# Kernel optimization log

Measured on AMD Instinct MI355X. Metric: run time of the kernel, lower is better.

The kernel has to match this reference:

```python
import jax, jax.numpy as jnp
import numpy as np

N_NODES = 100000
N_EDGES = 1600000
IN_DIM = 256
OUT_DIM = 128
SELF_LOOP_W = 2.0  # improved=True


def setup_inputs() -> dict:
    key = jax.random.key(0)
    ks = jax.random.split(key, 9)
    x = jax.random.normal(ks[0], (N_NODES, IN_DIM), dtype=jnp.float32)
    edge_index = jax.random.randint(ks[1], (2, N_EDGES), 0, N_NODES, dtype=jnp.int64)
    edge_weight = jax.random.uniform(ks[2], (N_EDGES,), dtype=jnp.float32)
    s1 = 1.0 / np.sqrt(IN_DIM)
    s2 = 1.0 / np.sqrt(OUT_DIM)
    W1 = jax.random.normal(ks[3], (IN_DIM, OUT_DIM), dtype=jnp.float32) * s1
    b1 = jnp.zeros((OUT_DIM,), dtype=jnp.float32)
    W_mu = jax.random.normal(ks[4], (OUT_DIM, OUT_DIM), dtype=jnp.float32) * s2
    b_mu = jnp.zeros((OUT_DIM,), dtype=jnp.float32)
    W_var = jax.random.normal(ks[5], (OUT_DIM, OUT_DIM), dtype=jnp.float32) * s2
    b_var = jnp.zeros((OUT_DIM,), dtype=jnp.float32)
    return {"x": x, "edge_index": edge_index, "edge_weight": edge_weight,
            "W1": W1, "b1": b1, "W_mu": W_mu, "b_mu": b_mu,
            "W_var": W_var, "b_var": b_var}


def _gcn_norm(edge_index, edge_weight, num_nodes):
    # add self loops with fill value 2.0 (improved=True), then symmetric norm
    loop = jnp.arange(num_nodes, dtype=edge_index.dtype)
    row = jnp.concatenate([edge_index[0], loop])
    col = jnp.concatenate([edge_index[1], loop])
    ew = jnp.concatenate([edge_weight,
                          jnp.full((num_nodes,), SELF_LOOP_W, dtype=edge_weight.dtype)])
    deg = jax.ops.segment_sum(ew, col, num_segments=num_nodes)
    dis = jnp.where(deg > 0, jax.lax.rsqrt(jnp.where(deg > 0, deg, 1.0)), 0.0)
    norm = dis[row] * ew * dis[col]
    return row, col, norm


def _gcn_conv(x, row, col, norm, W, b, num_nodes):
    xw = x @ W                      # [N, out]
    msg = xw[row] * norm[:, None]   # [E+N, out] per-edge messages
    out = jax.ops.segment_sum(msg, col, num_segments=num_nodes)
    return out + b


def reference(x, edge_index, edge_weight, W1, b1, W_mu, b_mu, W_var, b_var):
    n = x.shape[0]
    row, col, norm = _gcn_norm(edge_index, edge_weight, n)
    feat = jax.nn.relu(_gcn_conv(x, row, col, norm, W1, b1, n))
    mu = _gcn_conv(feat, row, col, norm, W_mu, b_mu, n)
    var = _gcn_conv(feat, row, col, norm, W_var, b_var, n)
    return (mu, var)
```

## Files before the change

kernel.cpp:

```cpp
#include <hip/hip_runtime.h>
#include <hip/hip_bf16.h>

#define CDIV(a,b) (((a)+(b)-1)/(b))

typedef __attribute__((ext_vector_type(8))) short short8;
typedef __attribute__((ext_vector_type(4))) float f32x4;

static __device__ inline short f2bf(float f) {
    union { __hip_bfloat16 h; short s; } u;
    u.h = __float2bfloat16(f);
    return u.s;
}
static __device__ inline ushort f2bfu(float f) { return (ushort)f2bf(f); }
static __device__ inline float bfu_lo(uint v) { return __uint_as_float(v << 16); }
static __device__ inline float bfu_hi(uint v) { return __uint_as_float(v & 0xffff0000u); }


__global__ __launch_bounds__(512) void k_init(const float* __restrict__ W1,
                                              short* __restrict__ W1t,
                                              const float* __restrict__ Wmu,
                                              const float* __restrict__ Wvar,
                                              short* __restrict__ Wcat) {
    int i = blockIdx.x * 512 + threadIdx.x;
    if (i < 128 * 256) {
        int k = i % 256, col = i / 256;
        W1t[i] = f2bf(W1[(size_t)k * 128 + col]);
    } else if (i < 2 * 128 * 256) {
        int j = i - 128 * 256;
        int k = j & 127, col = j >> 7;
        float v = (col < 128) ? Wmu[(size_t)k * 128 + col] : Wvar[(size_t)k * 128 + (col - 128)];
        Wcat[j] = f2bf(v);
    }
}


__global__ __launch_bounds__(512) void k_bhist(const int* __restrict__ coli,
                                               int* __restrict__ bhist,
                                               int E, int chunk, int nbk) {
    __shared__ int h[256];
    int b = blockIdx.x, t = threadIdx.x, nblk = gridDim.x;
    for (int i = t; i < nbk; i += 512) h[i] = 0;
    __syncthreads();
    int e0 = b * chunk, e1 = min(E, e0 + chunk);
    for (int e = e0 + t; e < e1; e += 512)
        atomicAdd(&h[coli[e] >> 9], 1);
    __syncthreads();
    for (int i = t; i < nbk; i += 512)
        bhist[i * nblk + b] = h[i];
}

__global__ __launch_bounds__(256) void kscanA(const int* __restrict__ in,
                                              int* __restrict__ out,
                                              int* __restrict__ part, int n) {
    int t = threadIdx.x;
    int base = blockIdx.x * 1024 + t * 4;
    int v0 = (base + 0 < n) ? in[base + 0] : 0;
    int v1 = (base + 1 < n) ? in[base + 1] : 0;
    int v2 = (base + 2 < n) ? in[base + 2] : 0;
    int v3 = (base + 3 < n) ? in[base + 3] : 0;
    int tsum = v0 + v1 + v2 + v3;
    int lane = t & 63, wv = t >> 6;
    int val = tsum;
    #pragma unroll
    for (int d = 1; d < 64; d <<= 1) {
        int u = __shfl_up(val, d, 64);
        if (lane >= d) val += u;
    }
    __shared__ int ws[4];
    if (lane == 63) ws[wv] = val;
    __syncthreads();
    int woff = 0;
    #pragma unroll
    for (int i = 0; i < 4; ++i) if (i < wv) woff += ws[i];
    int excl = woff + val - tsum;
    if (base + 0 < n) out[base + 0] = excl;  excl += v0;
    if (base + 1 < n) out[base + 1] = excl;  excl += v1;
    if (base + 2 < n) out[base + 2] = excl;  excl += v2;
    if (base + 3 < n) out[base + 3] = excl;
    if (t == 255) part[blockIdx.x] = woff + val;
}

__global__ __launch_bounds__(128) void kscanB(int* part, int nb) {
    int t = threadIdx.x;
    int v = (t < nb) ? part[t] : 0;
    int lane = t & 63, wv = t >> 6;
    int val = v;
    #pragma unroll
    for (int d = 1; d < 64; d <<= 1) {
        int u = __shfl_up(val, d, 64);
        if (lane >= d) val += u;
    }
    __shared__ int ws[2];
    if (lane == 63) ws[wv] = val;
    __syncthreads();
    int woff = (wv == 1) ? ws[0] : 0;
    if (t < nb) part[t] = woff + val - v;
}

__global__ __launch_bounds__(256) void kscanC(int* __restrict__ out,
                                              const int* __restrict__ part, int n) {
    int i = blockIdx.x * 256 + threadIdx.x;
    if (i < n) out[i] += part[i >> 10];
}

__global__ __launch_bounds__(512) void k_bucket(const int* __restrict__ rowi,
                                                const int* __restrict__ coli,
                                                const float* __restrict__ ew,
                                                const int* __restrict__ excl,
                                                int2* __restrict__ bxw,
                                                int E, int chunk, int nbk) {
    __shared__ int cur[256];
    int b = blockIdx.x, t = threadIdx.x, nblk = gridDim.x;
    for (int i = t; i < nbk; i += 512) cur[i] = 0;
    __syncthreads();
    int e0 = b * chunk, e1 = min(E, e0 + chunk);
    for (int e = e0 + t; e < e1; e += 512) {
        int c = coli[e];
        int bk = c >> 9;
        int pos = excl[bk * nblk + b] + atomicAdd(&cur[bk], 1);
        bxw[pos] = make_int2(((c & 511) << 17) | rowi[e], __float_as_int(ew[e]));
    }
}

__global__ __launch_bounds__(512) void k_fine2(const int2* __restrict__ bxw,
                                               const int* __restrict__ excl,
                                               int* __restrict__ row_ptr,
                                               float* __restrict__ dis,
                                               int E, int nblk, int n) {
    __shared__ int cnt[512], ews[512];
    int bk = blockIdx.x, t = threadIdx.x;
    cnt[t] = 0; ews[t] = 0;
    __syncthreads();
    int s0 = excl[bk * nblk];
    int s1 = (bk + 1 < gridDim.x) ? excl[(bk + 1) * nblk] : E;
    for (int p = s0 + t; p < s1; p += 512) {
        int2 u = bxw[p];
        int cl = u.x >> 17;
        atomicAdd(&cnt[cl], 1);
        int q = (int)(__int_as_float(u.y) * 16777216.0f + 0.5f);
        atomicAdd(&ews[cl], q);
    }
    __syncthreads();
    int v = cnt[t];
    int lane = t & 63, wv = t >> 6;
    int val = v;
    #pragma unroll
    for (int d = 1; d < 64; d <<= 1) {
        int u = __shfl_up(val, d, 64);
        if (lane >= d) val += u;
    }
    __shared__ int ws2[8];
    if (lane == 63) ws2[wv] = val;
    __syncthreads();
    int woff = 0;
    #pragma unroll
    for (int i = 0; i < 8; ++i) if (i < wv) woff += ws2[i];
    int lexcl = woff + val - v;
    int c = bk * 512 + t;
    if (c < n) {
        row_ptr[c] = s0 + lexcl;
        dis[c] = rsqrtf(2.0f + (float)ews[t] * (1.0f / 16777216.0f));
    }
    if (bk == 0 && t == 0) row_ptr[n] = E;
}

__global__ __launch_bounds__(512) void k_place(const int2* __restrict__ bxw,
                                               const int* __restrict__ excl,
                                               const int* __restrict__ row_ptr,
                                               const float* __restrict__ dis,
                                               int2* __restrict__ csr,
                                               int E, int nblk, int n) {
    __shared__ int cur[512];
    int bk = blockIdx.x, t = threadIdx.x;
    cur[t] = 0;
    __syncthreads();
    int s0 = excl[bk * nblk];
    int s1 = (bk + 1 < gridDim.x) ? excl[(bk + 1) * nblk] : E;
    int cbase = bk * 512;
    for (int p = s0 + t; p < s1; p += 512) {
        int2 u = bxw[p];
        int cl = u.x >> 17, r = u.x & 0x1FFFF;
        int pos = row_ptr[cbase + cl] + atomicAdd(&cur[cl], 1);
        csr[pos] = make_int2(r, __float_as_int(dis[r] * __int_as_float(u.y)));
    }
}


__global__ __launch_bounds__(512) void k_gemm1(const float* __restrict__ A,
                                               const short* __restrict__ Bt,
                                               ushort* __restrict__ C, int n) {
    const int K = 256, KH = 128;
    __shared__ short Blds[128 * KH];
    int t = threadIdx.x;

    int wave = t >> 6, lane = t & 63;
    int lg = lane >> 4, lr = lane & 15;
    long row_base = (long)blockIdx.x * 256 + wave * 32;

    long ra0 = row_base + lr;      if (ra0 > n - 1) ra0 = n - 1;
    long ra1 = row_base + 16 + lr; if (ra1 > n - 1) ra1 = n - 1;

    f32x4 acc[2][8];
    #pragma unroll
    for (int i = 0; i < 2; ++i)
        #pragma unroll
        for (int j = 0; j < 8; ++j) acc[i][j] = (f32x4){0.f, 0.f, 0.f, 0.f};

    const float* pa0 = A + ra0 * K + lg * 8;
    const float* pa1 = A + ra1 * K + lg * 8;

    #pragma unroll
    for (int p = 0; p < 2; ++p) {
        if (p) __syncthreads();
        const int CHK = KH / 8;
        for (int c = t; c < 128 * CHK; c += 512) {
            int colw = c / CHK;
            int kb  = (c % CHK) * 16;
            int dst = colw * (KH * 2) + (kb ^ ((colw & 7) << 4));
            *(float4*)((char*)Blds + dst) =
                *(const float4*)((const char*)Bt + (size_t)colw * (K * 2) + p * (KH * 2) + kb);
        }
        __syncthreads();

        for (int k0 = 0; k0 < KH; k0 += 32) {
            int kg = p * KH + k0;
            float4 x0 = *(const float4*)(pa0 + kg);
            float4 x1 = *(const float4*)(pa0 + kg + 4);
            float4 y0 = *(const float4*)(pa1 + kg);
            float4 y1 = *(const float4*)(pa1 + kg + 4);
            short8 a0, a1;
            a0[0]=f2bf(x0.x); a0[1]=f2bf(x0.y); a0[2]=f2bf(x0.z); a0[3]=f2bf(x0.w);
            a0[4]=f2bf(x1.x); a0[5]=f2bf(x1.y); a0[6]=f2bf(x1.z); a0[7]=f2bf(x1.w);
            a1[0]=f2bf(y0.x); a1[1]=f2bf(y0.y); a1[2]=f2bf(y0.z); a1[3]=f2bf(y0.w);
            a1[4]=f2bf(y1.x); a1[5]=f2bf(y1.y); a1[6]=f2bf(y1.z); a1[7]=f2bf(y1.w);

            int kb = (k0 + lg * 8) * 2;
            #pragma unroll
            for (int cb = 0; cb < 8; ++cb) {
                int colm = cb * 16 + lr;
                short8 bfr = *(short8*)((char*)Blds + colm * (KH * 2) + (kb ^ ((colm & 7) << 4)));
                acc[0][cb] = __builtin_amdgcn_mfma_f32_16x16x32_bf16(a0, bfr, acc[0][cb], 0, 0, 0);
                acc[1][cb] = __builtin_amdgcn_mfma_f32_16x16x32_bf16(a1, bfr, acc[1][cb], 0, 0, 0);
            }
        }
    }

    #pragma unroll
    for (int rf = 0; rf < 2; ++rf) {
        #pragma unroll
        for (int cb = 0; cb < 8; ++cb) {
            int colm = cb * 16 + lr;
            #pragma unroll
            for (int r = 0; r < 4; ++r) {
                long row = row_base + rf * 16 + lg * 4 + r;
                if (row < n) C[row * 128 + colm] = f2bfu(acc[rf][cb][r]);
            }
        }
    }
}


template<int OUTMODE>
__global__ __launch_bounds__(128) void k_agg(const uint2* __restrict__ src,
                                             const int* __restrict__ row_ptr,
                                             const int2* __restrict__ csr,
                                             const float* __restrict__ dis,
                                             const float* __restrict__ bias,
                                             uint2* __restrict__ dst, int n) {
    int wid = (blockIdx.x * 128 + threadIdx.x) >> 6;
    int lane = threadIdx.x & 63;
    int hb = lane >> 5, lc = lane & 31;
    if (wid >= n) return;
    int e0 = row_ptr[wid], e1 = row_ptr[wid + 1];

    float p00=0.f,p01=0.f,p02=0.f,p03=0.f;
    float p10=0.f,p11=0.f,p12=0.f,p13=0.f;
    float p20=0.f,p21=0.f,p22=0.f,p23=0.f;
    float p30=0.f,p31=0.f,p32=0.f,p33=0.f;

    int e = e0;
    for (; e + 7 < e1; e += 8) {
        int2 c0 = csr[e     + hb];
        int2 c1 = csr[e + 2 + hb];
        int2 c2 = csr[e + 4 + hb];
        int2 c3 = csr[e + 6 + hb];
        uint2 v0 = src[(size_t)c0.x * 32 + lc];
        uint2 v1 = src[(size_t)c1.x * 32 + lc];
        uint2 v2 = src[(size_t)c2.x * 32 + lc];
        uint2 v3 = src[(size_t)c3.x * 32 + lc];
        float w0 = __int_as_float(c0.y), w1 = __int_as_float(c1.y);
        float w2 = __int_as_float(c2.y), w3 = __int_as_float(c3.y);
        p00 += w0 * bfu_lo(v0.x); p01 += w0 * bfu_hi(v0.x);
        p02 += w0 * bfu_lo(v0.y); p03 += w0 * bfu_hi(v0.y);
        p10 += w1 * bfu_lo(v1.x); p11 += w1 * bfu_hi(v1.x);
        p12 += w1 * bfu_lo(v1.y); p13 += w1 * bfu_hi(v1.y);
        p20 += w2 * bfu_lo(v2.x); p21 += w2 * bfu_hi(v2.x);
        p22 += w2 * bfu_lo(v2.y); p23 += w2 * bfu_hi(v2.y);
        p30 += w3 * bfu_lo(v3.x); p31 += w3 * bfu_hi(v3.x);
        p32 += w3 * bfu_lo(v3.y); p33 += w3 * bfu_hi(v3.y);
    }
    for (; e + 1 < e1; e += 2) {
        int2 c = csr[e + hb];
        uint2 v = src[(size_t)c.x * 32 + lc];
        float w = __int_as_float(c.y);
        p00 += w * bfu_lo(v.x); p01 += w * bfu_hi(v.x);
        p02 += w * bfu_lo(v.y); p03 += w * bfu_hi(v.y);
    }
    if (e < e1 && hb == 0) {
        int2 c = csr[e];
        uint2 v = src[(size_t)c.x * 32 + lc];
        float w = __int_as_float(c.y);
        p10 += w * bfu_lo(v.x); p11 += w * bfu_hi(v.x);
        p12 += w * bfu_lo(v.y); p13 += w * bfu_hi(v.y);
    }

    float x0 = (p00 + p10) + (p20 + p30);
    float x1 = (p01 + p11) + (p21 + p31);
    float x2 = (p02 + p12) + (p22 + p32);
    float x3 = (p03 + p13) + (p23 + p33);
    x0 = x0 + __shfl_xor(x0, 32);
    x1 = x1 + __shfl_xor(x1, 32);
    x2 = x2 + __shfl_xor(x2, 32);
    x3 = x3 + __shfl_xor(x3, 32);

    float dc = dis[wid];
    uint2 sv = src[(size_t)wid * 32 + lc];
    float sw = 2.f * dc * dc;
    float o0 = dc * x0 + sw * bfu_lo(sv.x);
    float o1 = dc * x1 + sw * bfu_hi(sv.x);
    float o2 = dc * x2 + sw * bfu_lo(sv.y);
    float o3 = dc * x3 + sw * bfu_hi(sv.y);
    if constexpr (OUTMODE == 0) {
        float4 bv = *(const float4*)(bias + lc * 4);
        o0 += bv.x; o1 += bv.y; o2 += bv.z; o3 += bv.w;
        o0 = fmaxf(o0, 0.f); o1 = fmaxf(o1, 0.f);
        o2 = fmaxf(o2, 0.f); o3 = fmaxf(o3, 0.f);
    }
    if (hb == 0)
        dst[(size_t)wid * 32 + lc] =
            make_uint2((uint)f2bfu(o0) | ((uint)f2bfu(o1) << 16),
                       (uint)f2bfu(o2) | ((uint)f2bfu(o3) << 16));
}


__global__ __launch_bounds__(512) void k_gemm2(const short* __restrict__ A,
                                               const short* __restrict__ Bt,
                                               const float* __restrict__ bmu,
                                               const float* __restrict__ bvar,
                                               float* __restrict__ out,
                                               int n) {
    const int K = 128;
    __shared__ short Blds[256 * K];
    int t = threadIdx.x;

    const int CHK = K / 8;
    for (int c = t; c < 256 * CHK; c += 512) {
        int col = c / CHK;
        int kb  = (c % CHK) * 16;
        int dst = col * (K * 2) + (kb ^ ((col & 7) << 4));
        *(float4*)((char*)Blds + dst) =
            *(const float4*)((const char*)Bt + (size_t)col * (K * 2) + kb);
    }
    __syncthreads();

    int wave = t >> 6, lane = t & 63;
    int lg = lane >> 4, lr = lane & 15;
    int colbase = (wave & 1) * 128;
    long row_base = (long)blockIdx.x * 128 + (wave >> 1) * 32;

    long ra0 = row_base + lr;      if (ra0 > n - 1) ra0 = n - 1;
    long ra1 = row_base + 16 + lr; if (ra1 > n - 1) ra1 = n - 1;

    f32x4 acc[2][8];
    #pragma unroll
    for (int i = 0; i < 2; ++i)
        #pragma unroll
        for (int j = 0; j < 8; ++j) acc[i][j] = (f32x4){0.f, 0.f, 0.f, 0.f};

    const short* pa0 = A + ra0 * K + lg * 8;
    const short* pa1 = A + ra1 * K + lg * 8;

    #pragma unroll
    for (int k0 = 0; k0 < K; k0 += 32) {
        short8 a0 = *(const short8*)(pa0 + k0);
        short8 a1 = *(const short8*)(pa1 + k0);
        int kb = (k0 + lg * 8) * 2;
        #pragma unroll
        for (int cb = 0; cb < 8; ++cb) {
            int col = colbase + cb * 16 + lr;
            short8 b = *(short8*)((char*)Blds + col * (K * 2) + (kb ^ ((col & 7) << 4)));
            acc[0][cb] = __builtin_amdgcn_mfma_f32_16x16x32_bf16(a0, b, acc[0][cb], 0, 0, 0);
            acc[1][cb] = __builtin_amdgcn_mfma_f32_16x16x32_bf16(a1, b, acc[1][cb], 0, 0, 0);
        }
    }

    #pragma unroll
    for (int rf = 0; rf < 2; ++rf) {
        #pragma unroll
        for (int cb = 0; cb < 8; ++cb) {
            int colc = colbase + cb * 16 + lr;
            bool is_var = colc >= 128;
            int col = is_var ? colc - 128 : colc;
            float bv = is_var ? bvar[col] : bmu[col];
            size_t obase = is_var ? (size_t)n * 128 : 0;
            #pragma unroll
            for (int r = 0; r < 4; ++r) {
                long row = row_base + rf * 16 + lg * 4 + r;
                if (row < n)
                    __builtin_nontemporal_store(acc[rf][cb][r] + bv,
                                                &out[obase + (size_t)row * 128 + col]);
            }
        }
    }
}


extern "C" void kernel_launch(void* const* d_in, const int* in_sizes, int n_in,
                              void* d_out, int out_size, void* d_ws, size_t ws_size,
                              hipStream_t stream) {
    const float* x    = (const float*)d_in[0];
    const int*   ei   = (const int*)d_in[1];
    const float* ew   = (const float*)d_in[2];
    const float* W1   = (const float*)d_in[3];
    const float* b1   = (const float*)d_in[4];
    const float* Wmu  = (const float*)d_in[5];
    const float* bmu  = (const float*)d_in[6];
    const float* Wvar = (const float*)d_in[7];
    const float* bvar = (const float*)d_in[8];

    const int E = in_sizes[2];
    const int N = in_sizes[0] / 256;
    const int* rowi = ei;
    const int* coli = ei + E;

    char* base = (char*)d_ws;
    size_t off = 0;
    auto alloc = [&](size_t bytes) -> void* {
        void* p = base + off;
        off = (off + bytes + 511) & ~(size_t)511;
        return p;
    };
    const int NBLK = 256;
    const int nbk  = CDIV(N, 512);
    const int chunk = CDIV(E, NBLK);
    const int nh   = nbk * NBLK;

    int*   bhist   = (int*)  alloc((size_t)nh * 4);
    int*   excl    = (int*)  alloc((size_t)nh * 4);
    int*   part    = (int*)  alloc(256 * 4);
    int2*  bxw     = (int2*) alloc((size_t)E * 8);
    int*   row_ptr = (int*)  alloc((size_t)(N + 1) * 4);
    float* dis     = (float*)alloc((size_t)N * 4);
    int2*  csr     = (int2*) alloc((size_t)E * 8);
    uint*  xw      = (uint*) alloc((size_t)N * 64 * 4);
    uint*  feat    = (uint*) alloc((size_t)N * 64 * 4);
    short* W1t     = (short*)alloc((size_t)256 * 128 * 2);
    short* Wcat    = (short*)alloc((size_t)256 * 128 * 2);
    uint*  g       = xw;

    k_init<<<CDIV(2 * 128 * 256, 512), 512, 0, stream>>>(W1, W1t, Wmu, Wvar, Wcat);
    k_gemm1<<<CDIV(N, 256), 512, 0, stream>>>(x, W1t, (ushort*)xw, N);

    k_bhist<<<NBLK, 512, 0, stream>>>(coli, bhist, E, chunk, nbk);
    kscanA<<<CDIV(nh, 1024), 256, 0, stream>>>(bhist, excl, part, nh);
    kscanB<<<1, 128, 0, stream>>>(part, CDIV(nh, 1024));
    kscanC<<<CDIV(nh, 256), 256, 0, stream>>>(excl, part, nh);
    k_bucket<<<NBLK, 512, 0, stream>>>(rowi, coli, ew, excl, bxw, E, chunk, nbk);
    k_fine2<<<nbk, 512, 0, stream>>>(bxw, excl, row_ptr, dis, E, NBLK, N);
    k_place<<<nbk, 512, 0, stream>>>(bxw, excl, row_ptr, dis, csr, E, NBLK, N);

    k_agg<0><<<CDIV(N * 64, 128), 128, 0, stream>>>((const uint2*)xw, row_ptr, csr, dis, b1, (uint2*)feat, N);
    k_agg<1><<<CDIV(N * 64, 128), 128, 0, stream>>>((const uint2*)feat, row_ptr, csr, dis, nullptr, (uint2*)g, N);
    k_gemm2<<<CDIV(N, 128), 512, 0, stream>>>((const short*)g, Wcat, bmu, bvar, (float*)d_out, N);
}
```

Before: 264.1 us.

## Fuse gemm1 with edge histogram and drop scan fixup kernel

Merges the first GEMM and the destination-bucket histogram into one horizontally fused launch, with extra blocks doing the histogram in the GEMM's LDS. The separate kscanC pass is removed by having k_bucket, k_fine2 and k_place add the block partial sums on the fly. The histogram/bucket block count is also halved from 256 to 128. Together these cut two launches and let the histogram overlap with the GEMM, at the cost of extra part[] reads in three kernels and longer per-block edge chunks.

```diff
diff --git a/kernel.cpp b/kernel.cpp
--- a/kernel.cpp
+++ b/kernel.cpp
@@ -34,20 +34,96 @@
 }
 
 
-__global__ __launch_bounds__(512) void k_bhist(const int* __restrict__ coli,
-                                               int* __restrict__ bhist,
-                                               int E, int chunk, int nbk) {
-    __shared__ int h[256];
-    int b = blockIdx.x, t = threadIdx.x, nblk = gridDim.x;
-    for (int i = t; i < nbk; i += 512) h[i] = 0;
-    __syncthreads();
-    int e0 = b * chunk, e1 = min(E, e0 + chunk);
-    for (int e = e0 + t; e < e1; e += 512)
-        atomicAdd(&h[coli[e] >> 9], 1);
-    __syncthreads();
-    for (int i = t; i < nbk; i += 512)
-        bhist[i * nblk + b] = h[i];
-}
+__global__ __launch_bounds__(512) void k_fat(const float* __restrict__ A,
+                                             const short* __restrict__ Bt,
+                                             ushort* __restrict__ C, int n, int nGB,
+                                             const int* __restrict__ coli,
+                                             int* __restrict__ bhist,
+                                             int E, int chunkBH, int nbk, int NBH) {
+    const int K = 256, KH = 128;
+    __shared__ short Blds[128 * KH];
+    int t = threadIdx.x;
+
+    if (blockIdx.x >= nGB) {
+        int* h = (int*)Blds;
+        int b = blockIdx.x - nGB;
+        for (int i = t; i < nbk; i += 512) h[i] = 0;
+        __syncthreads();
+        int e0 = b * chunkBH, e1 = min(E, e0 + chunkBH);
+        for (int e = e0 + t; e < e1; e += 512)
+            atomicAdd(&h[coli[e] >> 9], 1);
+        __syncthreads();
+        for (int i = t; i < nbk; i += 512)
+            bhist[i * NBH + b] = h[i];
+        return;
+    }
+
+    int wave = t >> 6, lane = t & 63;
+    int lg = lane >> 4, lr = lane & 15;
+    long row_base = (long)blockIdx.x * 256 + wave * 32;
+
+    long ra0 = row_base + lr;      if (ra0 > n - 1) ra0 = n - 1;
+    long ra1 = row_base + 16 + lr; if (ra1 > n - 1) ra1 = n - 1;
+
+    f32x4 acc[2][8];
+    #pragma unroll
+    for (int i = 0; i < 2; ++i)
+        #pragma unroll
+        for (int j = 0; j < 8; ++j) acc[i][j] = (f32x4){0.f, 0.f, 0.f, 0.f};
+
+    const float* pa0 = A + ra0 * K + lg * 8;
+    const float* pa1 = A + ra1 * K + lg * 8;
+
+    #pragma unroll
+    for (int p = 0; p < 2; ++p) {
+        if (p) __syncthreads();
+        const int CHK = KH / 8;
+        for (int c = t; c < 128 * CHK; c += 512) {
+            int colw = c / CHK;
+            int kb  = (c % CHK) * 16;
+            int dst = colw * (KH * 2) + (kb ^ ((colw & 7) << 4));
+            *(float4*)((char*)Blds + dst) =
+                *(const float4*)((const char*)Bt + (size_t)colw * (K * 2) + p * (KH * 2) + kb);
+        }
+        __syncthreads();
+
+        for (int k0 = 0; k0 < KH; k0 += 32) {
+            int kg = p * KH + k0;
+            float4 x0 = *(const float4*)(pa0 + kg);
+            float4 x1 = *(const float4*)(pa0 + kg + 4);
+            float4 y0 = *(const float4*)(pa1 + kg);
+            float4 y1 = *(const float4*)(pa1 + kg + 4);
+            short8 a0, a1;
+            a0[0]=f2bf(x0.x); a0[1]=f2bf(x0.y); a0[2]=f2bf(x0.z); a0[3]=f2bf(x0.w);
+            a0[4]=f2bf(x1.x); a0[5]=f2bf(x1.y); a0[6]=f2bf(x1.z); a0[7]=f2bf(x1.w);
+            a1[0]=f2bf(y0.x); a1[1]=f2bf(y0.y); a1[2]=f2bf(y0.z); a1[3]=f2bf(y0.w);
+            a1[4]=f2bf(y1.x); a1[5]=f2bf(y1.y); a1[6]=f2bf(y1.z); a1[7]=f2bf(y1.w);
+
+            int kb = (k0 + lg * 8) * 2;
+            #pragma unroll
+            for (int cb = 0; cb < 8; ++cb) {
+                int colm = cb * 16 + lr;
+                short8 bfr = *(short8*)((char*)Blds + colm * (KH * 2) + (kb ^ ((colm & 7) << 4)));
+                acc[0][cb] = __builtin_amdgcn_mfma_f32_16x16x32_bf16(a0, bfr, acc[0][cb], 0, 0, 0);
+                acc[1][cb] = __builtin_amdgcn_mfma_f32_16x16x32_bf16(a1, bfr, acc[1][cb], 0, 0, 0);
+            }
+        }
+    }
+
+    #pragma unroll
+    for (int rf = 0; rf < 2; ++rf) {
+        #pragma unroll
+        for (int cb = 0; cb < 8; ++cb) {
+            int colm = cb * 16 + lr;
+            #pragma unroll
+            for (int r = 0; r < 4; ++r) {
+                long row = row_base + rf * 16 + lg * 4 + r;
+                if (row < n) C[row * 128 + colm] = f2bfu(acc[rf][cb][r]);
+            }
+        }
+    }
+}
+
 
 __global__ __launch_bounds__(256) void kscanA(const int* __restrict__ in,
                                               int* __restrict__ out,
@@ -97,16 +173,11 @@
     if (t < nb) part[t] = woff + val - v;
 }
 
-__global__ __launch_bounds__(256) void kscanC(int* __restrict__ out,
-                                              const int* __restrict__ part, int n) {
-    int i = blockIdx.x * 256 + threadIdx.x;
-    if (i < n) out[i] += part[i >> 10];
-}
-
 __global__ __launch_bounds__(512) void k_bucket(const int* __restrict__ rowi,
                                                 const int* __restrict__ coli,
                                                 const float* __restrict__ ew,
                                                 const int* __restrict__ excl,
+                                                const int* __restrict__ part,
                                                 int2* __restrict__ bxw,
                                                 int E, int chunk, int nbk) {
     __shared__ int cur[256];
@@ -117,13 +188,15 @@
     for (int e = e0 + t; e < e1; e += 512) {
         int c = coli[e];
         int bk = c >> 9;
-        int pos = excl[bk * nblk + b] + atomicAdd(&cur[bk], 1);
+        int idx = bk * nblk + b;
+        int pos = excl[idx] + part[idx >> 10] + atomicAdd(&cur[bk], 1);
         bxw[pos] = make_int2(((c & 511) << 17) | rowi[e], __float_as_int(ew[e]));
     }
 }
 
 __global__ __launch_bounds__(512) void k_fine2(const int2* __restrict__ bxw,
                                                const int* __restrict__ excl,
+                                               const int* __restrict__ part,
                                                int* __restrict__ row_ptr,
                                                float* __restrict__ dis,
                                                int E, int nblk, int n) {
@@ -131,8 +204,13 @@
     int bk = blockIdx.x, t = threadIdx.x;
     cnt[t] = 0; ews[t] = 0;
     __syncthreads();
-    int s0 = excl[bk * nblk];
-    int s1 = (bk + 1 < gridDim.x) ? excl[(bk + 1) * nblk] : E;
+    int i0 = bk * nblk;
+    int s0 = excl[i0] + part[i0 >> 10];
+    int s1 = E;
+    if (bk + 1 < gridDim.x) {
+        int i1 = (bk + 1) * nblk;
+        s1 = excl[i1] + part[i1 >> 10];
+    }
     for (int p = s0 + t; p < s1; p += 512) {
         int2 u = bxw[p];
         int cl = u.x >> 17;
@@ -166,6 +244,7 @@
 
 __global__ __launch_bounds__(512) void k_place(const int2* __restrict__ bxw,
                                                const int* __restrict__ excl,
+                                               const int* __restrict__ part,
                                                const int* __restrict__ row_ptr,
                                                const float* __restrict__ dis,
                                                int2* __restrict__ csr,
@@ -174,88 +253,19 @@
     int bk = blockIdx.x, t = threadIdx.x;
     cur[t] = 0;
     __syncthreads();
-    int s0 = excl[bk * nblk];
-    int s1 = (bk + 1 < gridDim.x) ? excl[(bk + 1) * nblk] : E;
+    int i0 = bk * nblk;
+    int s0 = excl[i0] + part[i0 >> 10];
+    int s1 = E;
+    if (bk + 1 < gridDim.x) {
+        int i1 = (bk + 1) * nblk;
+        s1 = excl[i1] + part[i1 >> 10];
+    }
     int cbase = bk * 512;
     for (int p = s0 + t; p < s1; p += 512) {
         int2 u = bxw[p];
         int cl = u.x >> 17, r = u.x & 0x1FFFF;
         int pos = row_ptr[cbase + cl] + atomicAdd(&cur[cl], 1);
         csr[pos] = make_int2(r, __float_as_int(dis[r] * __int_as_float(u.y)));
-    }
-}
-
-
-__global__ __launch_bounds__(512) void k_gemm1(const float* __restrict__ A,
-                                               const short* __restrict__ Bt,
-                                               ushort* __restrict__ C, int n) {
-    const int K = 256, KH = 128;
-    __shared__ short Blds[128 * KH];
-    int t = threadIdx.x;
-
-    int wave = t >> 6, lane = t & 63;
-    int lg = lane >> 4, lr = lane & 15;
-    long row_base = (long)blockIdx.x * 256 + wave * 32;
-
-    long ra0 = row_base + lr;      if (ra0 > n - 1) ra0 = n - 1;
-    long ra1 = row_base + 16 + lr; if (ra1 > n - 1) ra1 = n - 1;
-
-    f32x4 acc[2][8];
-    #pragma unroll
-    for (int i = 0; i < 2; ++i)
-        #pragma unroll
-        for (int j = 0; j < 8; ++j) acc[i][j] = (f32x4){0.f, 0.f, 0.f, 0.f};
-
-    const float* pa0 = A + ra0 * K + lg * 8;
-    const float* pa1 = A + ra1 * K + lg * 8;
-
-    #pragma unroll
-    for (int p = 0; p < 2; ++p) {
-        if (p) __syncthreads();
-        const int CHK = KH / 8;
-        for (int c = t; c < 128 * CHK; c += 512) {
-            int colw = c / CHK;
-            int kb  = (c % CHK) * 16;
-            int dst = colw * (KH * 2) + (kb ^ ((colw & 7) << 4));
-            *(float4*)((char*)Blds + dst) =
-                *(const float4*)((const char*)Bt + (size_t)colw * (K * 2) + p * (KH * 2) + kb);
-        }
-        __syncthreads();
-
-        for (int k0 = 0; k0 < KH; k0 += 32) {
-            int kg = p * KH + k0;
-            float4 x0 = *(const float4*)(pa0 + kg);
-            float4 x1 = *(const float4*)(pa0 + kg + 4);
-            float4 y0 = *(const float4*)(pa1 + kg);
-            float4 y1 = *(const float4*)(pa1 + kg + 4);
-            short8 a0, a1;
-            a0[0]=f2bf(x0.x); a0[1]=f2bf(x0.y); a0[2]=f2bf(x0.z); a0[3]=f2bf(x0.w);
-            a0[4]=f2bf(x1.x); a0[5]=f2bf(x1.y); a0[6]=f2bf(x1.z); a0[7]=f2bf(x1.w);
-            a1[0]=f2bf(y0.x); a1[1]=f2bf(y0.y); a1[2]=f2bf(y0.z); a1[3]=f2bf(y0.w);
-            a1[4]=f2bf(y1.x); a1[5]=f2bf(y1.y); a1[6]=f2bf(y1.z); a1[7]=f2bf(y1.w);
-
-            int kb = (k0 + lg * 8) * 2;
-            #pragma unroll
-            for (int cb = 0; cb < 8; ++cb) {
-                int colm = cb * 16 + lr;
-                short8 bfr = *(short8*)((char*)Blds + colm * (KH * 2) + (kb ^ ((colm & 7) << 4)));
-                acc[0][cb] = __builtin_amdgcn_mfma_f32_16x16x32_bf16(a0, bfr, acc[0][cb], 0, 0, 0);
-                acc[1][cb] = __builtin_amdgcn_mfma_f32_16x16x32_bf16(a1, bfr, acc[1][cb], 0, 0, 0);
-            }
-        }
-    }
-
-    #pragma unroll
-    for (int rf = 0; rf < 2; ++rf) {
-        #pragma unroll
-        for (int cb = 0; cb < 8; ++cb) {
-            int colm = cb * 16 + lr;
-            #pragma unroll
-            for (int r = 0; r < 4; ++r) {
-                long row = row_base + rf * 16 + lg * 4 + r;
-                if (row < n) C[row * 128 + colm] = f2bfu(acc[rf][cb][r]);
-            }
-        }
     }
 }
 
@@ -440,10 +450,11 @@
         off = (off + bytes + 511) & ~(size_t)511;
         return p;
     };
-    const int NBLK = 256;
+    const int NBH  = 128;
     const int nbk  = CDIV(N, 512);
-    const int chunk = CDIV(E, NBLK);
-    const int nh   = nbk * NBLK;
+    const int nh   = nbk * NBH;
+    const int nGB  = CDIV(N, 256);
+    const int chunkBH = CDIV(E, NBH);
 
     int*   bhist   = (int*)  alloc((size_t)nh * 4);
     int*   excl    = (int*)  alloc((size_t)nh * 4);
@@ -459,15 +470,15 @@
     uint*  g       = xw;
 
     k_init<<<CDIV(2 * 128 * 256, 512), 512, 0, stream>>>(W1, W1t, Wmu, Wvar, Wcat);
-    k_gemm1<<<CDIV(N, 256), 512, 0, stream>>>(x, W1t, (ushort*)xw, N);
-
-    k_bhist<<<NBLK, 512, 0, stream>>>(coli, bhist, E, chunk, nbk);
+
+    k_fat<<<nGB + NBH, 512, 0, stream>>>(x, W1t, (ushort*)xw, N, nGB,
+                                         coli, bhist, E, chunkBH, nbk, NBH);
+
     kscanA<<<CDIV(nh, 1024), 256, 0, stream>>>(bhist, excl, part, nh);
     kscanB<<<1, 128, 0, stream>>>(part, CDIV(nh, 1024));
-    kscanC<<<CDIV(nh, 256), 256, 0, stream>>>(excl, part, nh);
-    k_bucket<<<NBLK, 512, 0, stream>>>(rowi, coli, ew, excl, bxw, E, chunk, nbk);
-    k_fine2<<<nbk, 512, 0, stream>>>(bxw, excl, row_ptr, dis, E, NBLK, N);
-    k_place<<<nbk, 512, 0, stream>>>(bxw, excl, row_ptr, dis, csr, E, NBLK, N);
+    k_bucket<<<NBH, 512, 0, stream>>>(rowi, coli, ew, excl, part, bxw, E, chunkBH, nbk);
+    k_fine2<<<nbk, 512, 0, stream>>>(bxw, excl, part, row_ptr, dis, E, NBH, N);
+    k_place<<<nbk, 512, 0, stream>>>(bxw, excl, part, row_ptr, dis, csr, E, NBH, N);
 
     k_agg<0><<<CDIV(N * 64, 128), 128, 0, stream>>>((const uint2*)xw, row_ptr, csr, dis, b1, (uint2*)feat, N);
     k_agg<1><<<CDIV(N * 64, 128), 128, 0, stream>>>((const uint2*)feat, row_ptr, csr, dis, nullptr, (uint2*)g, N);
```

Result: no change. 263.6 us (-0.2%).
